# Kernel tuning notes

Measured on AMD Instinct MI355X. Metric: run time of the kernel, lower is better.

The kernel has to match this reference:

```python
import jax, jax.numpy as jnp
import numpy as np

UNITS = 400
FEAT = 3


def setup_inputs() -> dict:
    key = jax.random.key(0)
    ks = jax.random.split(key, 9)
    s_in = 1.0 / np.sqrt(FEAT)
    s_h = 1.0 / np.sqrt(UNITS)
    return {
        "inputs": jax.random.normal(ks[0], (64, 1000, FEAT), dtype=jnp.float32),
        "W_x": jax.random.normal(ks[1], (FEAT, 4 * UNITS), dtype=jnp.float32) * s_in,
        "W_h": jax.random.normal(ks[2], (UNITS, 4 * UNITS), dtype=jnp.float32) * s_h,
        "b": jnp.zeros((4 * UNITS,), dtype=jnp.float32),
        "p_i": jax.random.normal(ks[3], (UNITS,), dtype=jnp.float32) * 0.1,
        "p_f": jax.random.normal(ks[4], (UNITS,), dtype=jnp.float32) * 0.1,
        "p_o": jax.random.normal(ks[5], (UNITS,), dtype=jnp.float32) * 0.1,
        "W_out": jax.random.normal(ks[6], (UNITS, FEAT), dtype=jnp.float32) * s_h,
        "b_out": jnp.zeros((FEAT,), dtype=jnp.float32),
    }


def reference(inputs, W_x, W_h, b, p_i, p_f, p_o, W_out, b_out):
    B, T, _ = inputs.shape
    # Precompute input projections for all timesteps: [B, T, 4U]
    x_proj = jnp.einsum("btf,fg->btg", inputs, W_x) + b

    def step(carry, xp_t):
        h, c = carry  # [B, U] each
        z = xp_t + h @ W_h  # [B, 4U]
        zi, zf, zg, zo = jnp.split(z, 4, axis=-1)
        i = jax.nn.sigmoid(zi + p_i * c)  # peephole on c_prev
        f = jax.nn.sigmoid(zf + p_f * c)
        g = jnp.tanh(zg)
        c_new = f * c + i * g
        o = jax.nn.sigmoid(zo + p_o * c_new)  # peephole on new c
        h_new = o * jnp.tanh(c_new)
        return (h_new, c_new), h_new

    h0 = jnp.zeros((B, UNITS), dtype=inputs.dtype)
    c0 = jnp.zeros((B, UNITS), dtype=inputs.dtype)
    # scan over time: x_proj transposed to [T, B, 4U]
    _, hs = jax.lax.scan(step, (h0, c0), jnp.swapaxes(x_proj, 0, 1))
    hs = jnp.swapaxes(hs, 0, 1)  # [B, T, U]
    return jnp.einsum("btu,uf->btf", hs, W_out) + b_out
```

## Files before the change

kernel.cpp:

```cpp
#include <hip/hip_runtime.h>
#include <hip/hip_bf16.h>
#include <stdint.h>

#define UNITS 400
#define GATES 1600
#define TLEN  1000
#define BATCH 64

#define NBLK 8
#define NGRP 32
#define BPG  2
#define UPB  50
#define CPB  200
#define KK   10
#define KCH  40

#define WBUF_OFF  0
#define WBUF_SZ   (NBLK*UNITS*CPB*4)
#define HBUF_OFF  (WBUF_OFF + WBUF_SZ)
#define HBUF_SZ   (2*BATCH*UNITS*8)
#define PART_OFF  (HBUF_OFF + HBUF_SZ)
#define PART_SZ   (NGRP*NBLK*BPG*3*TLEN*4)
#define WS_FULL   ((size_t)PART_OFF + PART_SZ)

__device__ __forceinline__ float sigmoid_(float x) {
    return 1.0f / (1.0f + __expf(-x));
}
__device__ __forceinline__ float tanh_(float x) {
    return 1.0f - 2.0f / (__expf(2.0f * x) + 1.0f);
}

__global__ void reorder_w(const float* __restrict__ W_h, float* __restrict__ wbuf) {
    int i = blockIdx.x * 256 + threadIdx.x;
    if (i >= NBLK * UNITS * CPB) return;
    int c = i % CPB;
    int k = (i / CPB) % UNITS;
    int j = i / (CPB * UNITS);
    int g = c / UPB, u2 = c % UPB;
    int col = g * UNITS + j * UPB + u2;
    wbuf[i] = W_h[k * GATES + col];
}

__global__ __launch_bounds__(512, 1) void lstm_mb(
    const float* __restrict__ x,
    const float* __restrict__ W_x,
    const float* __restrict__ bvec,
    const float* __restrict__ p_i,
    const float* __restrict__ p_f,
    const float* __restrict__ p_o,
    const float* __restrict__ W_out,
    const float* __restrict__ wbuf,
    unsigned long long* __restrict__ hbuf,
    float*       __restrict__ part,
    float*       __restrict__ out)
{
    const int gr  = blockIdx.x % NGRP;
    const int j   = blockIdx.x / NGRP;
    const int tid = threadIdx.x;

    __shared__ float hsh[BPG][UNITS];
    __shared__ float zpart[KK][BPG][CPB];
    __shared__ float wosh[UPB][3];

    const float* wslice = wbuf + (size_t)j * UNITS * CPB;

    const int kk = tid / 50, cq = tid % 50;
    const bool zrole = (tid < KK * 50);
    const int k0 = kk * KCH;

    const int gb = tid / UPB, gu = tid % UPB;
    const bool grole = (tid < BPG * UPB);

    const bool prole = (tid < UNITS) && (tid / UPB != j);
    const bool yrole = (tid >= 500) && (tid < 500 + BPG * 3);
    const int yb = (tid - 500) / 3, yf = (tid - 500) % 3;

    float4 wreg[KCH];
    if (zrole) {
        #pragma unroll
        for (int r = 0; r < KCH; ++r)
            wreg[r] = *(const float4*)&wslice[(size_t)(k0 + r) * CPB + cq * 4];
    }

    int unit = 0, batch = 0;
    float wxr[3][4], bb[4];
    float piu = 0.f, pfu = 0.f, pou = 0.f, cc = 0.f;
    if (grole) {
        unit  = j * UPB + gu;
        batch = gr * BPG + gb;
        #pragma unroll
        for (int g = 0; g < 4; ++g) {
            const int gcol = g * UNITS + unit;
            wxr[0][g] = W_x[0 * GATES + gcol];
            wxr[1][g] = W_x[1 * GATES + gcol];
            wxr[2][g] = W_x[2 * GATES + gcol];
            bb[g]     = bvec[gcol];
        }
        piu = p_i[unit]; pfu = p_f[unit]; pou = p_o[unit];
    }
    if (tid < UPB * 3) wosh[tid / 3][tid % 3] = W_out[(j * UPB + tid / 3) * 3 + (tid % 3)];

    if (tid < UNITS) { hsh[0][tid] = 0.f; hsh[1][tid] = 0.f; }
    __syncthreads();

    for (int t = 0; t < TLEN; ++t) {
        const int p = t & 1;

        if (zrole) {
            float4 a0 = {0,0,0,0}, a1 = a0;
            #pragma unroll
            for (int ro = 0; ro < KCH; ro += 4) {
                const float4 h0 = *(const float4*)&hsh[0][k0 + ro];
                const float4 h1 = *(const float4*)&hsh[1][k0 + ro];
                #pragma unroll
                for (int dr = 0; dr < 4; ++dr) {
                    const float4 w = wreg[ro + dr];
                    const float e0 = (dr==0)?h0.x:(dr==1)?h0.y:(dr==2)?h0.z:h0.w;
                    const float e1 = (dr==0)?h1.x:(dr==1)?h1.y:(dr==2)?h1.z:h1.w;
                    a0.x = fmaf(e0, w.x, a0.x); a0.y = fmaf(e0, w.y, a0.y);
                    a0.z = fmaf(e0, w.z, a0.z); a0.w = fmaf(e0, w.w, a0.w);
                    a1.x = fmaf(e1, w.x, a1.x); a1.y = fmaf(e1, w.y, a1.y);
                    a1.z = fmaf(e1, w.z, a1.z); a1.w = fmaf(e1, w.w, a1.w);
                }
            }
            *(float4*)&zpart[kk][0][cq * 4] = a0;
            *(float4*)&zpart[kk][1][cq * 4] = a1;
        } else if (yrole && t > 0) {
            float s = 0.f;
            #pragma unroll
            for (int u = 0; u < UPB; ++u)
                s += hsh[yb][j * UPB + u] * wosh[u][yf];
            part[(((size_t)(gr * NBLK + j) * BPG + yb) * 3 + yf) * TLEN + (t - 1)] = s;
        }
        __syncthreads();

        if (grole) {
            const float x0 = x[((size_t)batch * TLEN + t) * 3 + 0];
            const float x1 = x[((size_t)batch * TLEN + t) * 3 + 1];
            const float x2 = x[((size_t)batch * TLEN + t) * 3 + 2];
            float s[4];
            #pragma unroll
            for (int g = 0; g < 4; ++g) {
                float acc = fmaf(x0, wxr[0][g],
                            fmaf(x1, wxr[1][g],
                            fmaf(x2, wxr[2][g], bb[g])));
                #pragma unroll
                for (int q = 0; q < KK; ++q) acc += zpart[q][gb][g * UPB + gu];
                s[g] = acc;
            }
            const float ig = sigmoid_(fmaf(piu, cc, s[0]));
            const float fg = sigmoid_(fmaf(pfu, cc, s[1]));
            const float gg = tanh_(s[2]);
            const float cn = fmaf(fg, cc, ig * gg);
            const float og = sigmoid_(fmaf(pou, cn, s[3]));
            const float hn = og * tanh_(cn);
            cc = cn;
            hsh[gb][unit] = hn;
            const unsigned long long pkt =
                ((unsigned long long)(unsigned)(t + 1) << 32) |
                (unsigned long long)__float_as_uint(hn);
            __hip_atomic_store(&hbuf[(size_t)p * BATCH * UNITS + (size_t)batch * UNITS + unit],
                               pkt, __ATOMIC_RELAXED, __HIP_MEMORY_SCOPE_AGENT);
        }

        if (prole) {
            const unsigned want = (unsigned)(t + 1);
            const size_t base = (size_t)p * BATCH * UNITS
                              + (size_t)(gr * BPG) * UNITS + tid;
            unsigned long long v0, v1;
            for (;;) {
                v0 = __hip_atomic_load(&hbuf[base],
                                       __ATOMIC_RELAXED, __HIP_MEMORY_SCOPE_AGENT);
                v1 = __hip_atomic_load(&hbuf[base + UNITS],
                                       __ATOMIC_RELAXED, __HIP_MEMORY_SCOPE_AGENT);
                if ((unsigned)(v0 >> 32) == want && (unsigned)(v1 >> 32) == want) break;
                __builtin_amdgcn_s_sleep(2);
            }
            hsh[0][tid] = __uint_as_float((unsigned)v0);
            hsh[1][tid] = __uint_as_float((unsigned)v1);
        }
        __syncthreads();
    }

    if (yrole) {
        float s = 0.f;
        #pragma unroll
        for (int u = 0; u < UPB; ++u)
            s += hsh[yb][j * UPB + u] * wosh[u][yf];
        part[(((size_t)(gr * NBLK + j) * BPG + yb) * 3 + yf) * TLEN + (TLEN - 1)] = s;
    }
}

__global__ void finish_y(const float* __restrict__ part,
                         const float* __restrict__ b_out,
                         float* __restrict__ out) {
    int i = blockIdx.x * 256 + threadIdx.x;
    if (i >= BATCH * TLEN * 3) return;
    const int f = i % 3;
    const int bt = i / 3;
    const int t = bt % TLEN;
    const int b = bt / TLEN;
    const int gr = b / BPG, gb = b % BPG;
    float s = b_out[f];
    #pragma unroll
    for (int j = 0; j < NBLK; ++j)
        s += part[(((size_t)(gr * NBLK + j) * BPG + gb) * 3 + f) * TLEN + t];
    out[i] = s;
}

__global__ __launch_bounds__(512) void lstm_fused_fb(
    const float* __restrict__ x, const float* __restrict__ W_x,
    const float* __restrict__ W_h, const float* __restrict__ bvec,
    const float* __restrict__ p_i, const float* __restrict__ p_f,
    const float* __restrict__ p_o, const float* __restrict__ W_out,
    const float* __restrict__ b_out, float* __restrict__ out)
{
    const int b = blockIdx.x, tid = threadIdx.x;
    const int lane = tid & 63, wv = tid >> 6;
    __shared__ float hsh[UNITS], csh[UNITS], zsh[GATES], xb[3], red[8][3];
    const float4* Wh4 = (const float4*)W_h;
    const int g = tid;
    float4 wx0, wx1, wx2, bb;
    if (g < GATES/4) {
        const float4* Wx4 = (const float4*)W_x;
        wx0 = Wx4[0*400 + g]; wx1 = Wx4[1*400 + g]; wx2 = Wx4[2*400 + g];
        bb  = ((const float4*)bvec)[g];
    }
    float piu=0.f,pfu=0.f,pou=0.f,wo0=0.f,wo1=0.f,wo2=0.f;
    if (tid < UNITS) {
        piu=p_i[tid]; pfu=p_f[tid]; pou=p_o[tid];
        wo0=W_out[tid*3]; wo1=W_out[tid*3+1]; wo2=W_out[tid*3+2];
        hsh[tid]=0.f; csh[tid]=0.f;
    }
    const float bo = (tid<3)?b_out[tid]:0.f;
    const float* xrow = x + (size_t)b*TLEN*3;
    float* orow = out + (size_t)b*TLEN*3;
    for (int t=0;t<TLEN;++t){
        if (tid<3) xb[tid]=xrow[t*3+tid];
        __syncthreads();
        const float x0=xb[0],x1=xb[1],x2=xb[2];
        if (g < GATES/4){
            float4 acc;
            acc.x=fmaf(x0,wx0.x,fmaf(x1,wx1.x,fmaf(x2,wx2.x,bb.x)));
            acc.y=fmaf(x0,wx0.y,fmaf(x1,wx1.y,fmaf(x2,wx2.y,bb.y)));
            acc.z=fmaf(x0,wx0.z,fmaf(x1,wx1.z,fmaf(x2,wx2.z,bb.z)));
            acc.w=fmaf(x0,wx0.w,fmaf(x1,wx1.w,fmaf(x2,wx2.w,bb.w)));
            const float4* wp=Wh4+g;
            #pragma unroll 8
            for(int k=0;k<UNITS;++k){
                const float hk=hsh[k]; const float4 w=wp[(size_t)k*400];
                acc.x=fmaf(hk,w.x,acc.x); acc.y=fmaf(hk,w.y,acc.y);
                acc.z=fmaf(hk,w.z,acc.z); acc.w=fmaf(hk,w.w,acc.w);
            }
            ((float4*)zsh)[g]=acc;
        }
        __syncthreads();
        float s0=0.f,s1=0.f,s2=0.f;
        if (tid<UNITS){
            const float cc=csh[tid];
            const float zi=zsh[tid],zf=zsh[tid+UNITS],zg=zsh[tid+2*UNITS],zo=zsh[tid+3*UNITS];
            const float ig=sigmoid_(fmaf(piu,cc,zi));
            const float fg=sigmoid_(fmaf(pfu,cc,zf));
            const float gg=tanh_(zg);
            const float cn=fmaf(fg,cc,ig*gg);
            const float og=sigmoid_(fmaf(pou,cn,zo));
            const float hn=og*tanh_(cn);
            csh[tid]=cn; hsh[tid]=hn;
            s0=hn*wo0; s1=hn*wo1; s2=hn*wo2;
        }
        #pragma unroll
        for(int off=32;off;off>>=1){
            s0+=__shfl_down(s0,off); s1+=__shfl_down(s1,off); s2+=__shfl_down(s2,off);
        }
        if(lane==0){red[wv][0]=s0;red[wv][1]=s1;red[wv][2]=s2;}
        __syncthreads();
        if(tid<3){
            float r=bo;
            #pragma unroll
            for(int w2=0;w2<8;++w2) r+=red[w2][tid];
            orow[t*3+tid]=r;
        }
    }
}

extern "C" void kernel_launch(void* const* d_in, const int* in_sizes, int n_in,
                              void* d_out, int out_size, void* d_ws, size_t ws_size,
                              hipStream_t stream) {
    const float* x     = (const float*)d_in[0];
    const float* W_x   = (const float*)d_in[1];
    const float* W_h   = (const float*)d_in[2];
    const float* b     = (const float*)d_in[3];
    const float* p_i   = (const float*)d_in[4];
    const float* p_f   = (const float*)d_in[5];
    const float* p_o   = (const float*)d_in[6];
    const float* W_out = (const float*)d_in[7];
    const float* b_out = (const float*)d_in[8];
    float* out = (float*)d_out;

    if (ws_size < WS_FULL) {
        lstm_fused_fb<<<BATCH, 512, 0, stream>>>(x, W_x, W_h, b, p_i, p_f, p_o,
                                                 W_out, b_out, out);
        return;
    }

    uint8_t* ws = (uint8_t*)d_ws;
    float* wbuf = (float*)(ws + WBUF_OFF);
    unsigned long long* hbuf = (unsigned long long*)(ws + HBUF_OFF);
    float* part = (float*)(ws + PART_OFF);

    hipMemsetAsync(hbuf, 0, HBUF_SZ, stream);
    reorder_w<<<(NBLK * UNITS * CPB + 255) / 256, 256, 0, stream>>>(W_h, wbuf);
    lstm_mb<<<NGRP * NBLK, 512, 0, stream>>>(x, W_x, b, p_i, p_f, p_o,
                                             W_out, wbuf, hbuf, part, out);
    finish_y<<<(BATCH * TLEN * 3 + 255) / 256, 256, 0, stream>>>(part, b_out, out);
}
```

Before: 3.032 ms.

## Stream bf16 recurrent weights from global memory instead of holding fp32 in registers

The recurrent weight slice is now stored as bf16 in the workspace and read from global memory every timestep, instead of being kept as 160 fp32 registers per thread. This frees registers and halves the weight footprint, but adds per-step global/L2 traffic and bf16 rounding error in the recurrence. The x input loads are moved to a few dedicated threads that stage them in shared memory. A spin cap is added to the cross-block wait loop, so it cannot hang forever.

```diff
diff --git a/kernel.cpp b/kernel.cpp
--- a/kernel.cpp
+++ b/kernel.cpp
@@ -16,13 +16,15 @@
 #define KCH  40
 
 #define WBUF_OFF  0
-#define WBUF_SZ   (NBLK*UNITS*CPB*4)
+#define WBUF_SZ   (NBLK*UNITS*CPB*2)
 #define HBUF_OFF  (WBUF_OFF + WBUF_SZ)
 #define HBUF_SZ   (2*BATCH*UNITS*8)
 #define PART_OFF  (HBUF_OFF + HBUF_SZ)
 #define PART_SZ   (NGRP*NBLK*BPG*3*TLEN*4)
 #define WS_FULL   ((size_t)PART_OFF + PART_SZ)
 
+#define SPIN_CAP (1 << 20)
+
 __device__ __forceinline__ float sigmoid_(float x) {
     return 1.0f / (1.0f + __expf(-x));
 }
@@ -30,15 +32,14 @@
     return 1.0f - 2.0f / (__expf(2.0f * x) + 1.0f);
 }
 
-__global__ void reorder_w(const float* __restrict__ W_h, float* __restrict__ wbuf) {
+__global__ void reorder_w(const float* __restrict__ W_h, __hip_bfloat16* __restrict__ wbuf) {
     int i = blockIdx.x * 256 + threadIdx.x;
     if (i >= NBLK * UNITS * CPB) return;
     int c = i % CPB;
     int k = (i / CPB) % UNITS;
     int j = i / (CPB * UNITS);
-    int g = c / UPB, u2 = c % UPB;
-    int col = g * UNITS + j * UPB + u2;
-    wbuf[i] = W_h[k * GATES + col];
+    int col = (c / UPB) * UNITS + j * UPB + (c % UPB);
+    wbuf[i] = __float2bfloat16(W_h[k * GATES + col]);
 }
 
 __global__ __launch_bounds__(512, 1) void lstm_mb(
@@ -49,7 +50,7 @@
     const float* __restrict__ p_f,
     const float* __restrict__ p_o,
     const float* __restrict__ W_out,
-    const float* __restrict__ wbuf,
+    const __hip_bfloat16* __restrict__ wbuf,
     unsigned long long* __restrict__ hbuf,
     float*       __restrict__ part,
     float*       __restrict__ out)
@@ -61,8 +62,9 @@
     __shared__ float hsh[BPG][UNITS];
     __shared__ float zpart[KK][BPG][CPB];
     __shared__ float wosh[UPB][3];
-
-    const float* wslice = wbuf + (size_t)j * UNITS * CPB;
+    __shared__ float xsh[BPG][4];
+
+    const __hip_bfloat16* wsl = wbuf + (size_t)j * UNITS * CPB;
 
     const int kk = tid / 50, cq = tid % 50;
     const bool zrole = (tid < KK * 50);
@@ -74,13 +76,8 @@
     const bool prole = (tid < UNITS) && (tid / UPB != j);
     const bool yrole = (tid >= 500) && (tid < 500 + BPG * 3);
     const int yb = (tid - 500) / 3, yf = (tid - 500) % 3;
-
-    float4 wreg[KCH];
-    if (zrole) {
-        #pragma unroll
-        for (int r = 0; r < KCH; ++r)
-            wreg[r] = *(const float4*)&wslice[(size_t)(k0 + r) * CPB + cq * 4];
-    }
+    const bool xrole = (tid >= 500 + BPG * 3) && (tid < 500 + 2 * BPG * 3);
+    const int xb2 = (tid - 500 - BPG * 3) / 3, xf = (tid - 500 - BPG * 3) % 3;
 
     int unit = 0, batch = 0;
     float wxr[3][4], bb[4];
@@ -103,6 +100,16 @@
     if (tid < UNITS) { hsh[0][tid] = 0.f; hsh[1][tid] = 0.f; }
     __syncthreads();
 
+#define WROW(U, HE0, HE1) {                                                        \
+    const float w0 = __uint_as_float((U).x << 16);                                 \
+    const float w1 = __uint_as_float((U).x & 0xffff0000u);                         \
+    const float w2 = __uint_as_float((U).y << 16);                                 \
+    const float w3 = __uint_as_float((U).y & 0xffff0000u);                         \
+    a0.x = fmaf(HE0, w0, a0.x); a0.y = fmaf(HE0, w1, a0.y);                        \
+    a0.z = fmaf(HE0, w2, a0.z); a0.w = fmaf(HE0, w3, a0.w);                        \
+    a1.x = fmaf(HE1, w0, a1.x); a1.y = fmaf(HE1, w1, a1.y);                        \
+    a1.z = fmaf(HE1, w2, a1.z); a1.w = fmaf(HE1, w3, a1.w); }
+
     for (int t = 0; t < TLEN; ++t) {
         const int p = t & 1;
 
@@ -110,18 +117,17 @@
             float4 a0 = {0,0,0,0}, a1 = a0;
             #pragma unroll
             for (int ro = 0; ro < KCH; ro += 4) {
-                const float4 h0 = *(const float4*)&hsh[0][k0 + ro];
-                const float4 h1 = *(const float4*)&hsh[1][k0 + ro];
-                #pragma unroll
-                for (int dr = 0; dr < 4; ++dr) {
-                    const float4 w = wreg[ro + dr];
-                    const float e0 = (dr==0)?h0.x:(dr==1)?h0.y:(dr==2)?h0.z:h0.w;
-                    const float e1 = (dr==0)?h1.x:(dr==1)?h1.y:(dr==2)?h1.z:h1.w;
-                    a0.x = fmaf(e0, w.x, a0.x); a0.y = fmaf(e0, w.y, a0.y);
-                    a0.z = fmaf(e0, w.z, a0.z); a0.w = fmaf(e0, w.w, a0.w);
-                    a1.x = fmaf(e1, w.x, a1.x); a1.y = fmaf(e1, w.y, a1.y);
-                    a1.z = fmaf(e1, w.z, a1.z); a1.w = fmaf(e1, w.w, a1.w);
-                }
+                const int kr = k0 + ro;
+                const uint2 u0 = *(const uint2*)(wsl + (size_t)(kr + 0) * CPB + (cq << 2));
+                const uint2 u1 = *(const uint2*)(wsl + (size_t)(kr + 1) * CPB + (cq << 2));
+                const uint2 u2 = *(const uint2*)(wsl + (size_t)(kr + 2) * CPB + (cq << 2));
+                const uint2 u3 = *(const uint2*)(wsl + (size_t)(kr + 3) * CPB + (cq << 2));
+                const float4 h0 = *(const float4*)&hsh[0][kr];
+                const float4 h1 = *(const float4*)&hsh[1][kr];
+                WROW(u0, h0.x, h1.x)
+                WROW(u1, h0.y, h1.y)
+                WROW(u2, h0.z, h1.z)
+                WROW(u3, h0.w, h1.w)
             }
             *(float4*)&zpart[kk][0][cq * 4] = a0;
             *(float4*)&zpart[kk][1][cq * 4] = a1;
@@ -131,13 +137,13 @@
             for (int u = 0; u < UPB; ++u)
                 s += hsh[yb][j * UPB + u] * wosh[u][yf];
             part[(((size_t)(gr * NBLK + j) * BPG + yb) * 3 + yf) * TLEN + (t - 1)] = s;
+        } else if (xrole) {
+            xsh[xb2][xf] = x[((size_t)(gr * BPG + xb2) * TLEN + t) * 3 + xf];
         }
         __syncthreads();
 
         if (grole) {
-            const float x0 = x[((size_t)batch * TLEN + t) * 3 + 0];
-            const float x1 = x[((size_t)batch * TLEN + t) * 3 + 1];
-            const float x2 = x[((size_t)batch * TLEN + t) * 3 + 2];
+            const float x0 = xsh[gb][0], x1 = xsh[gb][1], x2 = xsh[gb][2];
             float s[4];
             #pragma unroll
             for (int g = 0; g < 4; ++g) {
@@ -168,12 +174,14 @@
             const size_t base = (size_t)p * BATCH * UNITS
                               + (size_t)(gr * BPG) * UNITS + tid;
             unsigned long long v0, v1;
+            int guard = 0;
             for (;;) {
                 v0 = __hip_atomic_load(&hbuf[base],
                                        __ATOMIC_RELAXED, __HIP_MEMORY_SCOPE_AGENT);
                 v1 = __hip_atomic_load(&hbuf[base + UNITS],
                                        __ATOMIC_RELAXED, __HIP_MEMORY_SCOPE_AGENT);
                 if ((unsigned)(v0 >> 32) == want && (unsigned)(v1 >> 32) == want) break;
+                if (++guard > SPIN_CAP) break;
                 __builtin_amdgcn_s_sleep(2);
             }
             hsh[0][tid] = __uint_as_float((unsigned)v0);
@@ -189,6 +197,7 @@
             s += hsh[yb][j * UPB + u] * wosh[u][yf];
         part[(((size_t)(gr * NBLK + j) * BPG + yb) * 3 + yf) * TLEN + (TLEN - 1)] = s;
     }
+#undef WROW
 }
 
 __global__ void finish_y(const float* __restrict__ part,
@@ -304,7 +313,7 @@
     }
 
     uint8_t* ws = (uint8_t*)d_ws;
-    float* wbuf = (float*)(ws + WBUF_OFF);
+    __hip_bfloat16* wbuf = (__hip_bfloat16*)(ws + WBUF_OFF);
     unsigned long long* hbuf = (unsigned long long*)(ws + HBUF_OFF);
     float* part = (float*)(ws + PART_OFF);
 
```

Measured after the change: 4.523 ms. 1.49x slower.

## Process four batches per group and stream recurrent weights from global memory

Applied to the files above, without the earlier changes.

Halves the number of batch groups so each block computes four batch rows per step, cutting the block count and the number of cross-block handoffs. Recurrent weights are now loaded from global memory every timestep, no longer held in registers, so they are reused across four batch accumulators. The per-step input is staged into shared memory by spare threads, and the exchange poll now has a spin cap. The trade-off is heavy repeated weight traffic from cache every step and twice the serial work per block.

```diff
diff --git a/kernel.cpp b/kernel.cpp
--- a/kernel.cpp
+++ b/kernel.cpp
@@ -8,8 +8,8 @@
 #define BATCH 64
 
 #define NBLK 8
-#define NGRP 32
-#define BPG  2
+#define NGRP 16
+#define BPG  4
 #define UPB  50
 #define CPB  200
 #define KK   10
@@ -23,6 +23,8 @@
 #define PART_SZ   (NGRP*NBLK*BPG*3*TLEN*4)
 #define WS_FULL   ((size_t)PART_OFF + PART_SZ)
 
+#define SPIN_CAP (1 << 20)
+
 __device__ __forceinline__ float sigmoid_(float x) {
     return 1.0f / (1.0f + __expf(-x));
 }
@@ -36,8 +38,7 @@
     int c = i % CPB;
     int k = (i / CPB) % UNITS;
     int j = i / (CPB * UNITS);
-    int g = c / UPB, u2 = c % UPB;
-    int col = g * UNITS + j * UPB + u2;
+    int col = (c / UPB) * UNITS + j * UPB + (c % UPB);
     wbuf[i] = W_h[k * GATES + col];
 }
 
@@ -61,6 +62,7 @@
     __shared__ float hsh[BPG][UNITS];
     __shared__ float zpart[KK][BPG][CPB];
     __shared__ float wosh[UPB][3];
+    __shared__ float xsh[BPG][4];
 
     const float* wslice = wbuf + (size_t)j * UNITS * CPB;
 
@@ -71,16 +73,13 @@
     const int gb = tid / UPB, gu = tid % UPB;
     const bool grole = (tid < BPG * UPB);
 
-    const bool prole = (tid < UNITS) && (tid / UPB != j);
-    const bool yrole = (tid >= 500) && (tid < 500 + BPG * 3);
-    const int yb = (tid - 500) / 3, yf = (tid - 500) % 3;
-
-    float4 wreg[KCH];
-    if (zrole) {
-        #pragma unroll
-        for (int r = 0; r < KCH; ++r)
-            wreg[r] = *(const float4*)&wslice[(size_t)(k0 + r) * CPB + cq * 4];
-    }
+    const int  idx = tid - 150;
+    const bool prole = (tid >= 150) && (idx < UNITS - UPB);
+    const int  pu = idx + (idx >= j * UPB ? UPB : 0);
+
+    const bool yrole = (tid >= 500);
+    const int yi = tid - 500;
+    const int yb = yi / 3, yf = yi % 3;
 
     int unit = 0, batch = 0;
     float wxr[3][4], bb[4];
@@ -100,44 +99,55 @@
     }
     if (tid < UPB * 3) wosh[tid / 3][tid % 3] = W_out[(j * UPB + tid / 3) * 3 + (tid % 3)];
 
-    if (tid < UNITS) { hsh[0][tid] = 0.f; hsh[1][tid] = 0.f; }
+    if (tid < UNITS) {
+        #pragma unroll
+        for (int b = 0; b < BPG; ++b) hsh[b][tid] = 0.f;
+    }
     __syncthreads();
+
+#define FMA4(A, s, W) \
+    A.x = fmaf(s, W.x, A.x); A.y = fmaf(s, W.y, A.y); \
+    A.z = fmaf(s, W.z, A.z); A.w = fmaf(s, W.w, A.w);
 
     for (int t = 0; t < TLEN; ++t) {
         const int p = t & 1;
 
         if (zrole) {
-            float4 a0 = {0,0,0,0}, a1 = a0;
+            float4 A0 = {0,0,0,0}, A1 = A0, A2 = A0, A3 = A0;
             #pragma unroll
             for (int ro = 0; ro < KCH; ro += 4) {
+                const float* wp = wslice + (size_t)(k0 + ro) * CPB + (cq << 2);
+                const float4 w0 = *(const float4*)(wp);
+                const float4 w1 = *(const float4*)(wp + CPB);
+                const float4 w2 = *(const float4*)(wp + 2 * CPB);
+                const float4 w3 = *(const float4*)(wp + 3 * CPB);
                 const float4 h0 = *(const float4*)&hsh[0][k0 + ro];
                 const float4 h1 = *(const float4*)&hsh[1][k0 + ro];
+                const float4 h2 = *(const float4*)&hsh[2][k0 + ro];
+                const float4 h3 = *(const float4*)&hsh[3][k0 + ro];
+                FMA4(A0, h0.x, w0) FMA4(A0, h0.y, w1) FMA4(A0, h0.z, w2) FMA4(A0, h0.w, w3)
+                FMA4(A1, h1.x, w0) FMA4(A1, h1.y, w1) FMA4(A1, h1.z, w2) FMA4(A1, h1.w, w3)
+                FMA4(A2, h2.x, w0) FMA4(A2, h2.y, w1) FMA4(A2, h2.z, w2) FMA4(A2, h2.w, w3)
+                FMA4(A3, h3.x, w0) FMA4(A3, h3.y, w1) FMA4(A3, h3.z, w2) FMA4(A3, h3.w, w3)
+            }
+            *(float4*)&zpart[kk][0][cq << 2] = A0;
+            *(float4*)&zpart[kk][1][cq << 2] = A1;
+            *(float4*)&zpart[kk][2][cq << 2] = A2;
+            *(float4*)&zpart[kk][3][cq << 2] = A3;
+        } else if (yrole) {
+            xsh[yb][yf] = x[((size_t)(gr * BPG + yb) * TLEN + t) * 3 + yf];
+            if (t > 0) {
+                float s = 0.f;
                 #pragma unroll
-                for (int dr = 0; dr < 4; ++dr) {
-                    const float4 w = wreg[ro + dr];
-                    const float e0 = (dr==0)?h0.x:(dr==1)?h0.y:(dr==2)?h0.z:h0.w;
-                    const float e1 = (dr==0)?h1.x:(dr==1)?h1.y:(dr==2)?h1.z:h1.w;
-                    a0.x = fmaf(e0, w.x, a0.x); a0.y = fmaf(e0, w.y, a0.y);
-                    a0.z = fmaf(e0, w.z, a0.z); a0.w = fmaf(e0, w.w, a0.w);
-                    a1.x = fmaf(e1, w.x, a1.x); a1.y = fmaf(e1, w.y, a1.y);
-                    a1.z = fmaf(e1, w.z, a1.z); a1.w = fmaf(e1, w.w, a1.w);
-                }
-            }
-            *(float4*)&zpart[kk][0][cq * 4] = a0;
-            *(float4*)&zpart[kk][1][cq * 4] = a1;
-        } else if (yrole && t > 0) {
-            float s = 0.f;
-            #pragma unroll
-            for (int u = 0; u < UPB; ++u)
-                s += hsh[yb][j * UPB + u] * wosh[u][yf];
-            part[(((size_t)(gr * NBLK + j) * BPG + yb) * 3 + yf) * TLEN + (t - 1)] = s;
+                for (int u = 0; u < UPB; ++u)
+                    s += hsh[yb][j * UPB + u] * wosh[u][yf];
+                part[(((size_t)(gr * NBLK + j) * BPG + yb) * 3 + yf) * TLEN + (t - 1)] = s;
+            }
         }
         __syncthreads();
 
         if (grole) {
-            const float x0 = x[((size_t)batch * TLEN + t) * 3 + 0];
-            const float x1 = x[((size_t)batch * TLEN + t) * 3 + 1];
-            const float x2 = x[((size_t)batch * TLEN + t) * 3 + 2];
+            const float x0 = xsh[gb][0], x1 = xsh[gb][1], x2 = xsh[gb][2];
             float s[4];
             #pragma unroll
             for (int g = 0; g < 4; ++g) {
@@ -166,18 +176,25 @@
         if (prole) {
             const unsigned want = (unsigned)(t + 1);
             const size_t base = (size_t)p * BATCH * UNITS
-                              + (size_t)(gr * BPG) * UNITS + tid;
-            unsigned long long v0, v1;
+                              + (size_t)(gr * BPG) * UNITS + pu;
+            unsigned long long v0, v1, v2, v3;
+            int guard = 0;
             for (;;) {
-                v0 = __hip_atomic_load(&hbuf[base],
-                                       __ATOMIC_RELAXED, __HIP_MEMORY_SCOPE_AGENT);
-                v1 = __hip_atomic_load(&hbuf[base + UNITS],
-                                       __ATOMIC_RELAXED, __HIP_MEMORY_SCOPE_AGENT);
-                if ((unsigned)(v0 >> 32) == want && (unsigned)(v1 >> 32) == want) break;
+                v0 = __hip_atomic_load(&hbuf[base + 0 * UNITS], __ATOMIC_RELAXED, __HIP_MEMORY_SCOPE_AGENT);
+                v1 = __hip_atomic_load(&hbuf[base + 1 * UNITS], __ATOMIC_RELAXED, __HIP_MEMORY_SCOPE_AGENT);
+                v2 = __hip_atomic_load(&hbuf[base + 2 * UNITS], __ATOMIC_RELAXED, __HIP_MEMORY_SCOPE_AGENT);
+                v3 = __hip_atomic_load(&hbuf[base + 3 * UNITS], __ATOMIC_RELAXED, __HIP_MEMORY_SCOPE_AGENT);
+                const unsigned ok =
+                    ((unsigned)(v0 >> 32) == want) & ((unsigned)(v1 >> 32) == want) &
+                    ((unsigned)(v2 >> 32) == want) & ((unsigned)(v3 >> 32) == want);
+                if (ok) break;
+                if (++guard > SPIN_CAP) break;
                 __builtin_amdgcn_s_sleep(2);
             }
-            hsh[0][tid] = __uint_as_float((unsigned)v0);
-            hsh[1][tid] = __uint_as_float((unsigned)v1);
+            hsh[0][pu] = __uint_as_float((unsigned)v0);
+            hsh[1][pu] = __uint_as_float((unsigned)v1);
+            hsh[2][pu] = __uint_as_float((unsigned)v2);
+            hsh[3][pu] = __uint_as_float((unsigned)v3);
         }
         __syncthreads();
     }
@@ -189,6 +206,7 @@
             s += hsh[yb][j * UPB + u] * wosh[u][yf];
         part[(((size_t)(gr * NBLK + j) * BPG + yb) * 3 + yf) * TLEN + (TLEN - 1)] = s;
     }
+#undef FMA4
 }
 
 __global__ void finish_y(const float* __restrict__ part,
```

Result: slower. 5.092 ms (+67.9%).

## Replace per-step barrier with per-slice LDS counters and double-buffered hidden state

Applied to the files above, without the earlier changes.

Each z-thread now polls the global hbuf slot for its own 50-unit slice and waits on a workgroup-local counter for that slice. This lets the matvec for a slice start as soon as that slice's h values arrive instead of waiting on a full block barrier, and one of the two __syncthreads per step is removed. Hidden state and partial sums are double-buffered by step parity, and the gate threads move to a dedicated thread range. W_h is now streamed from global/L2 each step instead of held in registers, which adds memory traffic. Spin loops carry a cap that could break silently and produce wrong results under contention.

```diff
diff --git a/kernel.cpp b/kernel.cpp
--- a/kernel.cpp
+++ b/kernel.cpp
@@ -12,8 +12,7 @@
 #define BPG  2
 #define UPB  50
 #define CPB  200
-#define KK   10
-#define KCH  40
+#define NSL  8
 
 #define WBUF_OFF  0
 #define WBUF_SZ   (NBLK*UNITS*CPB*4)
@@ -23,6 +22,8 @@
 #define PART_SZ   (NGRP*NBLK*BPG*3*TLEN*4)
 #define WS_FULL   ((size_t)PART_OFF + PART_SZ)
 
+#define SPIN_CAP (1 << 18)
+
 __device__ __forceinline__ float sigmoid_(float x) {
     return 1.0f / (1.0f + __expf(-x));
 }
@@ -36,8 +37,7 @@
     int c = i % CPB;
     int k = (i / CPB) % UNITS;
     int j = i / (CPB * UNITS);
-    int g = c / UPB, u2 = c % UPB;
-    int col = g * UNITS + j * UPB + u2;
+    int col = (c / UPB) * UNITS + j * UPB + (c % UPB);
     wbuf[i] = W_h[k * GATES + col];
 }
 
@@ -58,29 +58,23 @@
     const int j   = blockIdx.x / NGRP;
     const int tid = threadIdx.x;
 
-    __shared__ float hsh[BPG][UNITS];
-    __shared__ float zpart[KK][BPG][CPB];
+    __shared__ float hsh[2][BPG][UNITS];
+    __shared__ float zpart[2][NSL][BPG][CPB];
     __shared__ float wosh[UPB][3];
+    __shared__ unsigned cnt[2][NSL];
 
     const float* wslice = wbuf + (size_t)j * UNITS * CPB;
 
-    const int kk = tid / 50, cq = tid % 50;
-    const bool zrole = (tid < KK * 50);
-    const int k0 = kk * KCH;
-
-    const int gb = tid / UPB, gu = tid % UPB;
-    const bool grole = (tid < BPG * UPB);
-
-    const bool prole = (tid < UNITS) && (tid / UPB != j);
-    const bool yrole = (tid >= 500) && (tid < 500 + BPG * 3);
-    const int yb = (tid - 500) / 3, yf = (tid - 500) % 3;
-
-    float4 wreg[KCH];
-    if (zrole) {
-        #pragma unroll
-        for (int r = 0; r < KCH; ++r)
-            wreg[r] = *(const float4*)&wslice[(size_t)(k0 + r) * CPB + cq * 4];
-    }
+    const bool zrole = (tid < 400);
+    const int  kk = tid / UPB, cq = tid % UPB;
+    const int  zunit = kk * UPB + cq;
+    const unsigned TGT = (kk == j) ? 100u : 50u;
+
+    const bool grole = (tid >= 400) && (tid < 500);
+    const int  gb = (tid - 400) / UPB, gu = (tid - 400) % UPB;
+
+    const bool yrole = (tid >= 500) && (tid < 506);
+    const int  yb = (tid - 500) / 3, yf = (tid - 500) % 3;
 
     int unit = 0, batch = 0;
     float wxr[3][4], bb[4];
@@ -100,52 +94,98 @@
     }
     if (tid < UPB * 3) wosh[tid / 3][tid % 3] = W_out[(j * UPB + tid / 3) * 3 + (tid % 3)];
 
-    if (tid < UNITS) { hsh[0][tid] = 0.f; hsh[1][tid] = 0.f; }
+    if (tid < UNITS) { hsh[0][0][tid] = 0.f; hsh[0][1][tid] = 0.f; }
+    if (tid < 2 * NSL) {
+        const int qq = tid / NSL, ss = tid % NSL;
+        cnt[qq][ss] = (qq == 0) ? ((ss == j) ? 100u : 50u) : 0u;
+    }
     __syncthreads();
 
     for (int t = 0; t < TLEN; ++t) {
-        const int p = t & 1;
+        const int q = t & 1;
+        const unsigned r = (unsigned)((t - q) / 2 + 1);
 
         if (zrole) {
-            float4 a0 = {0,0,0,0}, a1 = a0;
+            if (t > 0 && kk != j) {
+                const unsigned want = (unsigned)t;
+                const size_t base = (size_t)q * BATCH * UNITS
+                                  + (size_t)(gr * BPG) * UNITS + zunit;
+                unsigned long long v0, v1;
+                int gd = 0;
+                for (;;) {
+                    v0 = __hip_atomic_load(&hbuf[base], __ATOMIC_RELAXED, __HIP_MEMORY_SCOPE_AGENT);
+                    v1 = __hip_atomic_load(&hbuf[base + UNITS], __ATOMIC_RELAXED, __HIP_MEMORY_SCOPE_AGENT);
+                    if ((unsigned)(v0 >> 32) == want && (unsigned)(v1 >> 32) == want) break;
+                    if (++gd > SPIN_CAP) break;
+                    __builtin_amdgcn_s_sleep(1);
+                }
+                hsh[q][0][zunit] = __uint_as_float((unsigned)v0);
+                hsh[q][1][zunit] = __uint_as_float((unsigned)v1);
+                __hip_atomic_fetch_add(&cnt[q][kk], 1u,
+                                       __ATOMIC_RELEASE, __HIP_MEMORY_SCOPE_WORKGROUP);
+            }
+            {
+                const unsigned tgt = TGT * r;
+                int gd = 0;
+                while (__hip_atomic_load(&cnt[q][kk], __ATOMIC_ACQUIRE,
+                                         __HIP_MEMORY_SCOPE_WORKGROUP) < tgt) {
+                    if (++gd > SPIN_CAP) break;
+                    __builtin_amdgcn_s_sleep(1);
+                }
+            }
+            const int k0 = kk * UPB;
+            float4 A0 = {0, 0, 0, 0}, A1 = A0;
             #pragma unroll
-            for (int ro = 0; ro < KCH; ro += 4) {
-                const float4 h0 = *(const float4*)&hsh[0][k0 + ro];
-                const float4 h1 = *(const float4*)&hsh[1][k0 + ro];
-                #pragma unroll
-                for (int dr = 0; dr < 4; ++dr) {
-                    const float4 w = wreg[ro + dr];
-                    const float e0 = (dr==0)?h0.x:(dr==1)?h0.y:(dr==2)?h0.z:h0.w;
-                    const float e1 = (dr==0)?h1.x:(dr==1)?h1.y:(dr==2)?h1.z:h1.w;
-                    a0.x = fmaf(e0, w.x, a0.x); a0.y = fmaf(e0, w.y, a0.y);
-                    a0.z = fmaf(e0, w.z, a0.z); a0.w = fmaf(e0, w.w, a0.w);
-                    a1.x = fmaf(e1, w.x, a1.x); a1.y = fmaf(e1, w.y, a1.y);
-                    a1.z = fmaf(e1, w.z, a1.z); a1.w = fmaf(e1, w.w, a1.w);
-                }
-            }
-            *(float4*)&zpart[kk][0][cq * 4] = a0;
-            *(float4*)&zpart[kk][1][cq * 4] = a1;
+            for (int i = 0; i < UPB; i += 2) {
+                const float* wp = wslice + (size_t)(k0 + i) * CPB + (cq << 2);
+                const float4 w0 = *(const float4*)(wp);
+                const float4 w1 = *(const float4*)(wp + CPB);
+                const float2 h0 = *(const float2*)&hsh[q][0][k0 + i];
+                const float2 h1 = *(const float2*)&hsh[q][1][k0 + i];
+                A0.x = fmaf(h0.x, w0.x, A0.x); A0.y = fmaf(h0.x, w0.y, A0.y);
+                A0.z = fmaf(h0.x, w0.z, A0.z); A0.w = fmaf(h0.x, w0.w, A0.w);
+                A0.x = fmaf(h0.y, w1.x, A0.x); A0.y = fmaf(h0.y, w1.y, A0.y);
+                A0.z = fmaf(h0.y, w1.z, A0.z); A0.w = fmaf(h0.y, w1.w, A0.w);
+                A1.x = fmaf(h1.x, w0.x, A1.x); A1.y = fmaf(h1.x, w0.y, A1.y);
+                A1.z = fmaf(h1.x, w0.z, A1.z); A1.w = fmaf(h1.x, w0.w, A1.w);
+                A1.x = fmaf(h1.y, w1.x, A1.x); A1.y = fmaf(h1.y, w1.y, A1.y);
+                A1.z = fmaf(h1.y, w1.z, A1.z); A1.w = fmaf(h1.y, w1.w, A1.w);
+            }
+            *(float4*)&zpart[q][kk][0][cq << 2] = A0;
+            *(float4*)&zpart[q][kk][1][cq << 2] = A1;
+        } else if (grole) {
         } else if (yrole && t > 0) {
+            const unsigned tgt = 100u * r;
+            int gd = 0;
+            while (__hip_atomic_load(&cnt[q][j], __ATOMIC_ACQUIRE,
+                                     __HIP_MEMORY_SCOPE_WORKGROUP) < tgt) {
+                if (++gd > SPIN_CAP) break;
+                __builtin_amdgcn_s_sleep(1);
+            }
             float s = 0.f;
             #pragma unroll
             for (int u = 0; u < UPB; ++u)
-                s += hsh[yb][j * UPB + u] * wosh[u][yf];
+                s += hsh[q][yb][j * UPB + u] * wosh[u][yf];
             part[(((size_t)(gr * NBLK + j) * BPG + yb) * 3 + yf) * TLEN + (t - 1)] = s;
         }
+
+        float xv0 = 0.f, xv1 = 0.f, xv2 = 0.f;
+        if (grole) {
+            const float* xp = x + ((size_t)batch * TLEN + t) * 3;
+            xv0 = xp[0]; xv1 = xp[1]; xv2 = xp[2];
+        }
         __syncthreads();
 
         if (grole) {
-            const float x0 = x[((size_t)batch * TLEN + t) * 3 + 0];
-            const float x1 = x[((size_t)batch * TLEN + t) * 3 + 1];
-            const float x2 = x[((size_t)batch * TLEN + t) * 3 + 2];
             float s[4];
             #pragma unroll
             for (int g = 0; g < 4; ++g) {
-                float acc = fmaf(x0, wxr[0][g],
-                            fmaf(x1, wxr[1][g],
-                            fmaf(x2, wxr[2][g], bb[g])));
+                float acc = fmaf(xv0, wxr[0][g],
+                            fmaf(xv1, wxr[1][g],
+                            fmaf(xv2, wxr[2][g], bb[g])));
                 #pragma unroll
-                for (int q = 0; q < KK; ++q) acc += zpart[q][gb][g * UPB + gu];
+                for (int s8 = 0; s8 < NSL; ++s8)
+                    acc += zpart[q][s8][gb][g * UPB + gu];
                 s[g] = acc;
             }
             const float ig = sigmoid_(fmaf(piu, cc, s[0]));
@@ -155,38 +195,30 @@
             const float og = sigmoid_(fmaf(pou, cn, s[3]));
             const float hn = og * tanh_(cn);
             cc = cn;
-            hsh[gb][unit] = hn;
+            hsh[q ^ 1][gb][unit] = hn;
             const unsigned long long pkt =
                 ((unsigned long long)(unsigned)(t + 1) << 32) |
                 (unsigned long long)__float_as_uint(hn);
-            __hip_atomic_store(&hbuf[(size_t)p * BATCH * UNITS + (size_t)batch * UNITS + unit],
+            __hip_atomic_store(&hbuf[(size_t)(q ^ 1) * BATCH * UNITS
+                                     + (size_t)batch * UNITS + unit],
                                pkt, __ATOMIC_RELAXED, __HIP_MEMORY_SCOPE_AGENT);
-        }
-
-        if (prole) {
-            const unsigned want = (unsigned)(t + 1);
-            const size_t base = (size_t)p * BATCH * UNITS
-                              + (size_t)(gr * BPG) * UNITS + tid;
-            unsigned long long v0, v1;
-            for (;;) {
-                v0 = __hip_atomic_load(&hbuf[base],
-                                       __ATOMIC_RELAXED, __HIP_MEMORY_SCOPE_AGENT);
-                v1 = __hip_atomic_load(&hbuf[base + UNITS],
-                                       __ATOMIC_RELAXED, __HIP_MEMORY_SCOPE_AGENT);
-                if ((unsigned)(v0 >> 32) == want && (unsigned)(v1 >> 32) == want) break;
-                __builtin_amdgcn_s_sleep(2);
-            }
-            hsh[0][tid] = __uint_as_float((unsigned)v0);
-            hsh[1][tid] = __uint_as_float((unsigned)v1);
-        }
-        __syncthreads();
+            __hip_atomic_fetch_add(&cnt[q ^ 1][j], 1u,
+                                   __ATOMIC_RELEASE, __HIP_MEMORY_SCOPE_WORKGROUP);
+        }
     }
 
     if (yrole) {
+        const unsigned tgt = 100u * (unsigned)(TLEN / 2 + 1);
+        int gd = 0;
+        while (__hip_atomic_load(&cnt[0][j], __ATOMIC_ACQUIRE,
+                                 __HIP_MEMORY_SCOPE_WORKGROUP) < tgt) {
+            if (++gd > SPIN_CAP) break;
+            __builtin_amdgcn_s_sleep(1);
+        }
         float s = 0.f;
         #pragma unroll
         for (int u = 0; u < UPB; ++u)
-            s += hsh[yb][j * UPB + u] * wosh[u][yf];
+            s += hsh[0][yb][j * UPB + u] * wosh[u][yf];
         part[(((size_t)(gr * NBLK + j) * BPG + yb) * 3 + yf) * TLEN + (TLEN - 1)] = s;
     }
 }
```

Result: slower. 4.788 ms (+57.9%).
